# Optimization experiments

Hardware: AMD Instinct MI355X
Metric: run time of the kernel (lower is better)

## Reference

```python
import jax, jax.numpy as jnp
import numpy as np

H = 4096          # hidden_size
NH = 32           # num_attention_heads
NKV = 2           # multi_query_group_num (kv heads)
HD = 128          # kv_channels / head_dim
RD = 64           # rotary_dim = head_dim * rotary_percent(0.5)
T = 2048          # total tokens (single prefill sequence)
EPS = 1e-5        # layernorm_epsilon
ROPE_BASE = 10000.0


def setup_inputs() -> dict:
    key = jax.random.key(0)
    k0, k1, k2, k3 = jax.random.split(key, 4)
    qkv_out = (NH + 2 * NKV) * HD  # 4608
    return {
        "positions": jnp.arange(T, dtype=jnp.int32),
        "hidden_states": jax.random.normal(k0, (T, H), jnp.float32),
        "w_qkv": jax.random.normal(k1, (qkv_out, H), jnp.float32) * 0.02,
        "b_qkv": jax.random.normal(k2, (qkv_out,), jnp.float32) * 0.02,
        "w_dense": jax.random.normal(k3, (H, NH * HD), jnp.float32) * 0.02,
        "q_ln_w": jnp.ones((HD,), jnp.float32),
        "k_ln_w": jnp.ones((HD,), jnp.float32),
    }


def _rmsnorm(x, w):
    # per-head RMSNorm over head_dim
    return x * jax.lax.rsqrt(jnp.mean(x * x, axis=-1, keepdims=True) + EPS) * w


def _rope(x, positions):
    # partial rotary (first RD dims), interleaved GPT-J style (is_neox_style=False)
    inv_freq = 1.0 / (ROPE_BASE ** (jnp.arange(0, RD, 2, dtype=jnp.float32) / RD))
    ang = positions.astype(jnp.float32)[:, None] * inv_freq      # [T, RD//2]
    cos = jnp.cos(ang)[:, None, :]                               # [T, 1, RD//2]
    sin = jnp.sin(ang)[:, None, :]
    x_rot, x_pass = x[..., :RD], x[..., RD:]
    x1 = x_rot[..., 0::2]
    x2 = x_rot[..., 1::2]
    r1 = x1 * cos - x2 * sin
    r2 = x2 * cos + x1 * sin
    x_rot = jnp.stack([r1, r2], axis=-1).reshape(x.shape[:-1] + (RD,))
    return jnp.concatenate([x_rot, x_pass], axis=-1)


def reference(positions, hidden_states, w_qkv, b_qkv, w_dense, q_ln_w, k_ln_w):
    qkv = hidden_states @ w_qkv.T + b_qkv                        # [T, 4608]
    q_size, kv_size = NH * HD, NKV * HD
    q = qkv[:, :q_size].reshape(T, NH, HD)
    k = qkv[:, q_size:q_size + kv_size].reshape(T, NKV, HD)
    v = qkv[:, q_size + kv_size:].reshape(T, NKV, HD)
    # optional qk layernorm (RMSNorm since config.rmsnorm)
    q = _rmsnorm(q, q_ln_w)
    k = _rmsnorm(k, k_ln_w)
    # rotary embedding
    q = _rope(q, positions)
    k = _rope(k, positions)
    # GQA: expand kv heads to query heads
    group = NH // NKV
    k_exp = jnp.repeat(k, group, axis=1)                         # [T, NH, HD]
    v_exp = jnp.repeat(v, group, axis=1)
    scale = HD ** -0.5
    scores = jnp.einsum("thd,shd->hts", q, k_exp) * scale        # [NH, T, T]
    causal = jnp.tril(jnp.ones((T, T), dtype=bool))
    scores = jnp.where(causal[None, :, :], scores, jnp.finfo(scores.dtype).min)
    attn = jax.nn.softmax(scores, axis=-1)
    out = jnp.einsum("hts,shd->thd", attn, v_exp).reshape(T, NH * HD)
    return out @ w_dense.T                                       # [T, H]
```

## Files before the change

### kernel.cpp

```cpp
#include <hip/hip_runtime.h>
#include <cstdint>
#include <cstddef>

typedef short short4v __attribute__((ext_vector_type(4)));
typedef short short8v __attribute__((ext_vector_type(8)));
typedef float f32x4   __attribute__((ext_vector_type(4)));

#define T_LEN  2048
#define HDIM   4096
#define NHEADS 32
#define HEADD  128
#define QKVN   4608

static __device__ __forceinline__ short f2bf(float f) {
  __bf16 h = (__bf16)f;
  return __builtin_bit_cast(short, h);
}
static __device__ __forceinline__ float bf2f(short u) {
  return __builtin_bit_cast(float, ((unsigned int)(unsigned short)u) << 16);
}

static __device__ __forceinline__ void gload_lds16(const void* g, void* l) {
  __builtin_amdgcn_global_load_lds((const __attribute__((address_space(1))) void*)g,
                                   (__attribute__((address_space(3))) void*)l,
                                   16, 0, 0);
}

__global__ void cast_pair(const float* __restrict__ a, short* __restrict__ oa, int na4,
                          const float* __restrict__ b, short* __restrict__ ob, int nb4) {
  int idx = blockIdx.x * blockDim.x + threadIdx.x;
  int stride = gridDim.x * blockDim.x;
  const int ntot = na4 + nb4;
  for (int i = idx; i < ntot; i += stride) {
    const float4* src = (i < na4) ? ((const float4*)a + i) : ((const float4*)b + (i - na4));
    short4v* dst      = (i < na4) ? ((short4v*)oa + i)     : ((short4v*)ob + (i - na4));
    float4 v = *src;
    short4v o;
    o[0] = f2bf(v.x); o[1] = f2bf(v.y); o[2] = f2bf(v.z); o[3] = f2bf(v.w);
    *dst = o;
  }
}

__global__ void cast_f32_to_bf16(const float* __restrict__ in, short* __restrict__ out, int n4) {
  int idx = blockIdx.x * blockDim.x + threadIdx.x;
  int stride = gridDim.x * blockDim.x;
  const float4* in4 = (const float4*)in;
  short4v* out4 = (short4v*)out;
  for (int i = idx; i < n4; i += stride) {
    float4 v = in4[i];
    short4v o;
    o[0] = f2bf(v.x); o[1] = f2bf(v.y); o[2] = f2bf(v.z); o[3] = f2bf(v.w);
    out4[i] = o;
  }
}

template <int OUT_BF16>
__global__ __launch_bounds__(256, 2) void gemm_bt(
    const short* __restrict__ A,
    const short* __restrict__ B,
    const float* __restrict__ bias,
    void* __restrict__ Cout,
    int M, int N, int K)
{
  __shared__ short sA[128 * 64];
  __shared__ short sB[128 * 64];
  const int tid  = threadIdx.x;
  const int lane = tid & 63;
  const int wv   = tid >> 6;
  const int wr   = wv >> 1;
  const int wc   = wv & 1;

  const int nwg  = gridDim.x * gridDim.y;
  int wgid = blockIdx.y * gridDim.x + blockIdx.x;
  wgid = (wgid & 7) * (nwg >> 3) + (wgid >> 3);
  const int bn0 = (wgid / gridDim.y) * 128;
  const int bm0 = (wgid % gridDim.y) * 128;

  const int fr  = lane & 15;
  const int fkb = (lane >> 4) << 4;
  const int swz = (fr & 7) << 4;

  const int c_row  = tid >> 3;
  const int c_colb = (tid & 7) << 4;
  const int c_scol = (c_colb ^ ((c_row & 7) << 4)) >> 1;

  auto STAGE = [&](int kt) {
#pragma unroll
    for (int i = 0; i < 4; i++) {
      const int row = i * 32 + c_row;
      gload_lds16(A + (size_t)(bm0 + row) * K + kt + c_scol,
                  (char*)sA + (size_t)(i * 256 + wv * 64) * 16);
      gload_lds16(B + (size_t)(bn0 + row) * K + kt + c_scol,
                  (char*)sB + (size_t)(i * 256 + wv * 64) * 16);
    }
  };

  f32x4 zero = {0.f, 0.f, 0.f, 0.f};
  f32x4 acc[4][4];
#pragma unroll
  for (int m = 0; m < 4; m++)
#pragma unroll
    for (int n = 0; n < 4; n++) acc[m][n] = zero;

  for (int kt = 0; kt < K; kt += 64) {
    STAGE(kt);
    __syncthreads();
    const char* aB = (const char*)sA;
    const char* bB = (const char*)sB;
#pragma unroll
    for (int ks = 0; ks < 2; ks++) {
      short8v af[4], bfr[4];
#pragma unroll
      for (int m = 0; m < 4; m++) {
        const int row = wr * 64 + m * 16 + fr;
        af[m] = *(const short8v*)(aB + row * 128 + ((ks * 64 + fkb) ^ swz));
      }
#pragma unroll
      for (int n = 0; n < 4; n++) {
        const int row = wc * 64 + n * 16 + fr;
        bfr[n] = *(const short8v*)(bB + row * 128 + ((ks * 64 + fkb) ^ swz));
      }
#pragma unroll
      for (int m = 0; m < 4; m++)
#pragma unroll
        for (int n = 0; n < 4; n++)
          acc[m][n] = __builtin_amdgcn_mfma_f32_16x16x32_bf16(af[m], bfr[n], acc[m][n], 0, 0, 0);
    }
    __syncthreads();
  }

  const int rg = (lane >> 4) * 4;
#pragma unroll
  for (int m = 0; m < 4; m++) {
#pragma unroll
    for (int n = 0; n < 4; n++) {
      const int gcol = bn0 + wc * 64 + n * 16 + fr;
      const float bv = bias ? bias[gcol] : 0.0f;
#pragma unroll
      for (int j = 0; j < 4; j++) {
        const int grow = bm0 + wr * 64 + m * 16 + rg + j;
        const float v = acc[m][n][j] + bv;
        if (OUT_BF16)
          ((short*)Cout)[(size_t)grow * N + gcol] = f2bf(v);
        else
          ((float*)Cout)[(size_t)grow * N + gcol] = v;
      }
    }
  }
}

__global__ __launch_bounds__(256) void qkv_post_kernel(
    const short* __restrict__ qkvb,
    const int*   __restrict__ positions,
    const float* __restrict__ q_ln,
    const float* __restrict__ k_ln,
    short* __restrict__ Qb,
    short* __restrict__ Kb,
    short* __restrict__ Vt)
{
  const int t = blockIdx.x;
  const int h = blockIdx.y * 4 + (threadIdx.x >> 6);
  const int lane = threadIdx.x & 63;
  const unsigned int pk =
      ((const unsigned int*)(qkvb + (size_t)t * QKVN + h * HEADD))[lane];
  float x = bf2f((short)(pk & 0xffffu));
  float y = bf2f((short)(pk >> 16));

  if (h >= 34) {
    const int hv = h - 34;
    short* dst = Vt + ((size_t)hv * HEADD + 2 * lane) * T_LEN + t;
    dst[0]     = f2bf(x);
    dst[T_LEN] = f2bf(y);
    return;
  }

  float ss = x * x + y * y;
#pragma unroll
  for (int d = 32; d > 0; d >>= 1) ss += __shfl_xor(ss, d);
  const float r = rsqrtf(ss * (1.0f / 128.0f) + 1e-5f);
  const float* lnw = (h < 32) ? q_ln : k_ln;
  x = x * r * lnw[2 * lane];
  y = y * r * lnw[2 * lane + 1];

  if (lane < 32) {
    const float pos = (float)positions[t];
    const float ang = pos * powf(10000.0f, -(float)lane * (1.0f / 32.0f));
    const float c = cosf(ang), s = sinf(ang);
    const float r1 = x * c - y * s;
    const float r2 = y * c + x * s;
    x = r1; y = r2;
  }

  short* dst = (h < 32) ? (Qb + ((size_t)h * T_LEN + t) * HEADD + 2 * lane)
                        : (Kb + ((size_t)(h - 32) * T_LEN + t) * HEADD + 2 * lane);
  dst[0] = f2bf(x);
  dst[1] = f2bf(y);
}

__global__ __launch_bounds__(256, 2) void attn_kernel(
    const short* __restrict__ Qb,
    const short* __restrict__ Kb,
    const short* __restrict__ Vt,
    short* __restrict__ attn_out)
{
  __shared__ short Ks[2][64 * 128];
  __shared__ short Vs[2][128 * 64];
  __shared__ short pbuf[4][32 * 64];
  const int x    = blockIdx.x;
  const int h    = blockIdx.y;
  const int hkv  = h >> 4;
  const int tid  = threadIdx.x;
  const int lane = tid & 63;
  const int wv   = tid >> 6;
  const int qA   = x * 64 + wv * 16;
  const int qB   = (31 - x) * 64 + wv * 16;
  const int nt   = 32 - x;
  const int fr = lane & 15;
  const int fk = (lane >> 4) * 8;
  const int fkb = (lane >> 4) << 4;
  const int rg = (lane >> 4) * 4;
  const int swz = (fr & 7) << 4;

  const short* Kh = Kb + (size_t)hkv * T_LEN * HEADD;
  const short* Vh = Vt + (size_t)hkv * HEADD * T_LEN;

  short8v qf0[4], qf1[4];
  {
    const short* QrowA = Qb + ((size_t)h * T_LEN + qA + fr) * HEADD + fk;
    const short* QrowB = Qb + ((size_t)h * T_LEN + qB + fr) * HEADD + fk;
#pragma unroll
    for (int d0 = 0; d0 < 4; d0++) {
      qf0[d0] = *(const short8v*)(QrowA + d0 * 32);
      qf1[d0] = *(const short8v*)(QrowB + d0 * 32);
    }
  }

  float mrow[2][4], lrow[2][4];
#pragma unroll
  for (int g = 0; g < 2; g++)
#pragma unroll
    for (int j = 0; j < 4; j++) { mrow[g][j] = -1e30f; lrow[g][j] = 0.f; }
  f32x4 zero = {0.f, 0.f, 0.f, 0.f};
  f32x4 o[2][8];
#pragma unroll
  for (int g = 0; g < 2; g++)
#pragma unroll
    for (int d = 0; d < 8; d++) o[g][d] = zero;

  char* pb = (char*)&pbuf[wv][0];
  const float scale = 0.08838834764831845f;

  auto STAGE = [&](int b, int t) {
    const int s0 = t * 64;
#pragma unroll
    for (int i = 0; i < 4; i++) {
      const int c    = i * 256 + tid;
      const int row  = c >> 4;
      const int colb = (c & 15) << 4;
      const int scol = (colb ^ ((row & 7) << 4)) >> 1;
      gload_lds16(Kh + (size_t)(s0 + row) * HEADD + scol,
                  (char*)&Ks[b][0] + (size_t)(i * 256 + wv * 64) * 16);
    }
#pragma unroll
    for (int i = 0; i < 4; i++) {
      const int c    = i * 256 + tid;
      const int row  = c >> 3;
      const int colb = (c & 7) << 4;
      const int scol = (colb ^ ((row & 7) << 4)) >> 1;
      gload_lds16(Vh + (size_t)row * T_LEN + s0 + scol,
                  (char*)&Vs[b][0] + (size_t)(i * 256 + wv * 64) * 16);
    }
  };

  int cur = 0;
  STAGE(0, 0);
  __syncthreads();

  for (int t = 0; t < nt; ++t) {
    if (t + 1 < nt) STAGE(cur ^ 1, t + 1);
    const int s0 = t * 64;
    const bool dual = (t <= x);
    const char* KsB = (const char*)&Ks[cur][0];
    const char* VsB = (const char*)&Vs[cur][0];

    float scv0[4][4], scv1[4][4];
#pragma unroll
    for (int sub = 0; sub < 4; sub++) {
      const char* Kbase = KsB + (sub * 16 + fr) * 256;
      f32x4 a0 = zero, a1 = zero;
#pragma unroll
      for (int d0 = 0; d0 < 4; d0++) {
        short8v kf = *(const short8v*)(Kbase + ((d0 * 64 + fkb) ^ swz));
        a1 = __builtin_amdgcn_mfma_f32_16x16x32_bf16(qf1[d0], kf, a1, 0, 0, 0);
        if (dual) a0 = __builtin_amdgcn_mfma_f32_16x16x32_bf16(qf0[d0], kf, a0, 0, 0, 0);
      }
#pragma unroll
      for (int j = 0; j < 4; j++) {
        scv1[sub][j] = a1[j] * scale;
        scv0[sub][j] = a0[j] * scale;
      }
    }
    if (t == x) {
#pragma unroll
      for (int sub = 0; sub < 4; sub++) {
        const int colp = s0 + sub * 16 + fr;
#pragma unroll
        for (int j = 0; j < 4; j++)
          if (colp > qA + rg + j) scv0[sub][j] = -1e30f;
      }
    }
    if (t == nt - 1) {
#pragma unroll
      for (int sub = 0; sub < 4; sub++) {
        const int colp = s0 + sub * 16 + fr;
#pragma unroll
        for (int j = 0; j < 4; j++)
          if (colp > qB + rg + j) scv1[sub][j] = -1e30f;
      }
    }
    float pmax1[4], pmax0[4];
#pragma unroll
    for (int j = 0; j < 4; j++)
      pmax1[j] = fmaxf(fmaxf(scv1[0][j], scv1[1][j]), fmaxf(scv1[2][j], scv1[3][j]));
    float growth = -1e30f;
#pragma unroll
    for (int j = 0; j < 4; j++) growth = fmaxf(growth, pmax1[j] - mrow[1][j]);
    if (dual) {
#pragma unroll
      for (int j = 0; j < 4; j++) {
        pmax0[j] = fmaxf(fmaxf(scv0[0][j], scv0[1][j]), fmaxf(scv0[2][j], scv0[3][j]));
        growth = fmaxf(growth, pmax0[j] - mrow[0][j]);
      }
    }
    if (!__all(growth <= 8.0f)) {
#pragma unroll
      for (int j = 0; j < 4; j++) {
        float mx = pmax1[j];
#pragma unroll
        for (int d = 1; d < 16; d <<= 1) mx = fmaxf(mx, __shfl_xor(mx, d));
        const float mn = fmaxf(mrow[1][j], mx);
        const float c  = __expf(mrow[1][j] - mn);
        mrow[1][j] = mn;
        lrow[1][j] *= c;
#pragma unroll
        for (int df = 0; df < 8; df++) o[1][df][j] *= c;
      }
      if (dual) {
#pragma unroll
        for (int j = 0; j < 4; j++) {
          float mx = pmax0[j];
#pragma unroll
          for (int d = 1; d < 16; d <<= 1) mx = fmaxf(mx, __shfl_xor(mx, d));
          const float mn = fmaxf(mrow[0][j], mx);
          const float c  = __expf(mrow[0][j] - mn);
          mrow[0][j] = mn;
          lrow[0][j] *= c;
#pragma unroll
          for (int df = 0; df < 8; df++) o[0][df][j] *= c;
        }
      }
    }
#pragma unroll
    for (int j = 0; j < 4; j++) {
      const int rswz = ((rg + j) & 7) << 4;
      char* prb1 = pb + (16 + rg + j) * 128;
      float ps1 = 0.f;
#pragma unroll
      for (int sub = 0; sub < 4; sub++) {
        const float p = __expf(scv1[sub][j] - mrow[1][j]);
        ps1 += p;
        *(short*)(prb1 + ((((sub * 16 + fr) << 1)) ^ rswz)) = f2bf(p);
      }
      lrow[1][j] += ps1;
    }
    if (dual) {
#pragma unroll
      for (int j = 0; j < 4; j++) {
        const int rswz = ((rg + j) & 7) << 4;
        char* prb0 = pb + (rg + j) * 128;
        float ps0 = 0.f;
#pragma unroll
        for (int sub = 0; sub < 4; sub++) {
          const float p = __expf(scv0[sub][j] - mrow[0][j]);
          ps0 += p;
          *(short*)(prb0 + ((((sub * 16 + fr) << 1)) ^ rswz)) = f2bf(p);
        }
        lrow[0][j] += ps0;
      }
    }
    asm volatile("" ::: "memory");
    short8v pf1[2], pf0[2];
#pragma unroll
    for (int ks = 0; ks < 2; ks++) {
      pf1[ks] = *(const short8v*)(pb + (16 + fr) * 128 + ((ks * 64 + fkb) ^ swz));
      pf0[ks] = *(const short8v*)(pb + fr * 128 + ((ks * 64 + fkb) ^ swz));
    }
#pragma unroll
    for (int df = 0; df < 8; df++) {
      const char* Vbase = VsB + (df * 16 + fr) * 128;
      short8v vf0 = *(const short8v*)(Vbase + ((0 + fkb) ^ swz));
      short8v vf1 = *(const short8v*)(Vbase + ((64 + fkb) ^ swz));
      o[1][df] = __builtin_amdgcn_mfma_f32_16x16x32_bf16(pf1[0], vf0, o[1][df], 0, 0, 0);
      o[1][df] = __builtin_amdgcn_mfma_f32_16x16x32_bf16(pf1[1], vf1, o[1][df], 0, 0, 0);
      if (dual) {
        o[0][df] = __builtin_amdgcn_mfma_f32_16x16x32_bf16(pf0[0], vf0, o[0][df], 0, 0, 0);
        o[0][df] = __builtin_amdgcn_mfma_f32_16x16x32_bf16(pf0[1], vf1, o[0][df], 0, 0, 0);
      }
    }
    __syncthreads();
    cur ^= 1;
  }

#pragma unroll
  for (int g = 0; g < 2; g++)
#pragma unroll
    for (int j = 0; j < 4; j++) {
#pragma unroll
      for (int d = 1; d < 16; d <<= 1) lrow[g][j] += __shfl_xor(lrow[g][j], d);
    }
#pragma unroll
  for (int df = 0; df < 8; df++)
#pragma unroll
    for (int j = 0; j < 4; j++) {
      const float v0 = o[0][df][j] / lrow[0][j];
      attn_out[(size_t)(qA + rg + j) * HDIM + h * HEADD + df * 16 + fr] = f2bf(v0);
      const float v1 = o[1][df][j] / lrow[1][j];
      attn_out[(size_t)(qB + rg + j) * HDIM + h * HEADD + df * 16 + fr] = f2bf(v1);
    }
}

extern "C" void kernel_launch(void* const* d_in, const int* in_sizes, int n_in,
                              void* d_out, int out_size, void* d_ws, size_t ws_size,
                              hipStream_t stream) {
  (void)out_size; (void)ws_size;
  int ip = 0, ih = 1, iwq = 2, ib = 3, iwd = 4, il0 = 5, il1 = 6;
  if (n_in == 7) {
    int p = -1, hh = -1, wq = -1, b = -1, wd = -1, l0 = -1, l1 = -1, ok = 1;
    for (int i = 0; i < 7; i++) {
      switch (in_sizes[i]) {
        case 2048:     p  = i; break;
        case 8388608:  hh = i; break;
        case 18874368: wq = i; break;
        case 4608:     b  = i; break;
        case 16777216: wd = i; break;
        case 128:      if (l0 < 0) l0 = i; else l1 = i; break;
        default:       ok = 0; break;
      }
    }
    if (ok && p >= 0 && hh >= 0 && wq >= 0 && b >= 0 && wd >= 0 && l0 >= 0 && l1 >= 0) {
      ip = p; ih = hh; iwq = wq; ib = b; iwd = wd; il0 = l0; il1 = l1;
    }
  }

  const int*   positions = (const int*)d_in[ip];
  const float* hidden    = (const float*)d_in[ih];
  const float* w_qkv     = (const float*)d_in[iwq];
  const float* b_qkv     = (const float*)d_in[ib];
  const float* w_dense   = (const float*)d_in[iwd];
  const float* q_ln      = (const float*)d_in[il0];
  const float* k_ln      = (const float*)d_in[il1];

  char* ws = (char*)d_ws;
  short* Ahs   = (short*)(ws + 0);
  short* Qb    = (short*)(ws + 0);
  short* Wqkv  = (short*)(ws + (size_t)16777216);
  short* Kb    = (short*)(ws + (size_t)16777216);
  short* Vt    = (short*)(ws + (size_t)17825792);
  short* Wd    = (short*)(ws + (size_t)18874368);
  short* qkvb  = (short*)(ws + (size_t)54525952);
  short* attnb = (short*)(ws + (size_t)54525952);

  cast_pair<<<dim3(3072), dim3(256), 0, stream>>>(
      hidden, Ahs, (T_LEN * HDIM) / 4, w_qkv, Wqkv, (QKVN * HDIM) / 4);
  gemm_bt<1><<<dim3(QKVN / 128, T_LEN / 128), dim3(256), 0, stream>>>(
      Ahs, Wqkv, b_qkv, (void*)qkvb, T_LEN, QKVN, HDIM);
  qkv_post_kernel<<<dim3(T_LEN, 9), dim3(256), 0, stream>>>(
      qkvb, positions, q_ln, k_ln, Qb, Kb, Vt);
  cast_f32_to_bf16<<<dim3(2048), dim3(256), 0, stream>>>(w_dense, Wd, (HDIM * HDIM) / 4);
  attn_kernel<<<dim3(16, NHEADS), dim3(256), 0, stream>>>(Qb, Kb, Vt, attnb);
  gemm_bt<0><<<dim3(HDIM / 128, T_LEN / 128), dim3(256), 0, stream>>>(
      attnb, Wd, nullptr, d_out, T_LEN, HDIM, HDIM);
}
```

Before: 308.0 us.

## Fold dense-weight cast into attention launch and widen casts to 8 elements

New measurement: 310.4 us. About the same (+0.8%).

```diff
diff --git a/kernel.cpp b/kernel.cpp
--- a/kernel.cpp
+++ b/kernel.cpp
@@ -26,31 +26,23 @@
                                    16, 0, 0);
 }
 
-__global__ void cast_pair(const float* __restrict__ a, short* __restrict__ oa, int na4,
-                          const float* __restrict__ b, short* __restrict__ ob, int nb4) {
+static __device__ __forceinline__ short8v cvt8(float4 v0, float4 v1) {
+  short8v o;
+  o[0] = f2bf(v0.x); o[1] = f2bf(v0.y); o[2] = f2bf(v0.z); o[3] = f2bf(v0.w);
+  o[4] = f2bf(v1.x); o[5] = f2bf(v1.y); o[6] = f2bf(v1.z); o[7] = f2bf(v1.w);
+  return o;
+}
+
+__global__ void cast_pair(const float* __restrict__ a, short* __restrict__ oa, int na8,
+                          const float* __restrict__ b, short* __restrict__ ob, int nb8) {
   int idx = blockIdx.x * blockDim.x + threadIdx.x;
   int stride = gridDim.x * blockDim.x;
-  const int ntot = na4 + nb4;
+  const int ntot = na8 + nb8;
   for (int i = idx; i < ntot; i += stride) {
-    const float4* src = (i < na4) ? ((const float4*)a + i) : ((const float4*)b + (i - na4));
-    short4v* dst      = (i < na4) ? ((short4v*)oa + i)     : ((short4v*)ob + (i - na4));
-    float4 v = *src;
-    short4v o;
-    o[0] = f2bf(v.x); o[1] = f2bf(v.y); o[2] = f2bf(v.z); o[3] = f2bf(v.w);
-    *dst = o;
-  }
-}
-
-__global__ void cast_f32_to_bf16(const float* __restrict__ in, short* __restrict__ out, int n4) {
-  int idx = blockIdx.x * blockDim.x + threadIdx.x;
-  int stride = gridDim.x * blockDim.x;
-  const float4* in4 = (const float4*)in;
-  short4v* out4 = (short4v*)out;
-  for (int i = idx; i < n4; i += stride) {
-    float4 v = in4[i];
-    short4v o;
-    o[0] = f2bf(v.x); o[1] = f2bf(v.y); o[2] = f2bf(v.z); o[3] = f2bf(v.w);
-    out4[i] = o;
+    const float4* src = (i < na8) ? ((const float4*)a + 2 * (size_t)i)
+                                  : ((const float4*)b + 2 * (size_t)(i - na8));
+    short8v* dst      = (i < na8) ? ((short8v*)oa + i) : ((short8v*)ob + (i - na8));
+    *dst = cvt8(src[0], src[1]);
   }
 }
 
@@ -201,15 +193,28 @@
     const short* __restrict__ Qb,
     const short* __restrict__ Kb,
     const short* __restrict__ Vt,
-    short* __restrict__ attn_out)
+    short* __restrict__ attn_out,
+    const float* __restrict__ wd_src,
+    short* __restrict__ wd_dst)
 {
   __shared__ short Ks[2][64 * 128];
   __shared__ short Vs[2][128 * 64];
   __shared__ short pbuf[4][32 * 64];
+  const int tid  = threadIdx.x;
+
+  if (blockIdx.z == 1) {
+    const int bid = blockIdx.y * gridDim.x + blockIdx.x;
+    const int stride = gridDim.x * gridDim.y * 256;
+    for (int i = bid * 256 + tid; i < (HDIM * HDIM) / 8; i += stride) {
+      const float4* s = (const float4*)wd_src + 2 * (size_t)i;
+      ((short8v*)wd_dst)[i] = cvt8(s[0], s[1]);
+    }
+    return;
+  }
+
   const int x    = blockIdx.x;
   const int h    = blockIdx.y;
   const int hkv  = h >> 4;
-  const int tid  = threadIdx.x;
   const int lane = tid & 63;
   const int wv   = tid >> 6;
   const int qA   = x * 64 + wv * 16;
@@ -471,13 +476,13 @@
   short* attnb = (short*)(ws + (size_t)54525952);
 
   cast_pair<<<dim3(3072), dim3(256), 0, stream>>>(
-      hidden, Ahs, (T_LEN * HDIM) / 4, w_qkv, Wqkv, (QKVN * HDIM) / 4);
+      hidden, Ahs, (T_LEN * HDIM) / 8, w_qkv, Wqkv, (QKVN * HDIM) / 8);
   gemm_bt<1><<<dim3(QKVN / 128, T_LEN / 128), dim3(256), 0, stream>>>(
       Ahs, Wqkv, b_qkv, (void*)qkvb, T_LEN, QKVN, HDIM);
   qkv_post_kernel<<<dim3(T_LEN, 9), dim3(256), 0, stream>>>(
       qkvb, positions, q_ln, k_ln, Qb, Kb, Vt);
-  cast_f32_to_bf16<<<dim3(2048), dim3(256), 0, stream>>>(w_dense, Wd, (HDIM * HDIM) / 4);
-  attn_kernel<<<dim3(16, NHEADS), dim3(256), 0, stream>>>(Qb, Kb, Vt, attnb);
+  attn_kernel<<<dim3(16, NHEADS, 2), dim3(256), 0, stream>>>(
+      Qb, Kb, Vt, attnb, w_dense, Wd);
   gemm_bt<0><<<dim3(HDIM / 128, T_LEN / 128), dim3(256), 0, stream>>>(
       attnb, Wd, nullptr, d_out, T_LEN, HDIM, HDIM);
 }
```
